# Optimization experiments

Hardware: AMD Instinct MI355X
Metric: run time of the kernel (lower is better)

## Reference

```python
import jax, jax.numpy as jnp
import numpy as np

N = 100000   # nodes
M = N - 1    # tree edges (child -> parent)
EMB = 512    # embedding_size
ENC = 512    # encoder_size


def setup_inputs() -> dict:
    key = jax.random.key(0)
    ks = jax.random.split(key, 10)
    x = jax.random.normal(ks[0], (N, EMB), jnp.float32)
    h = jax.random.normal(ks[1], (N, ENC), jnp.float32)
    c = jax.random.normal(ks[2], (N, ENC), jnp.float32)
    child_idx = jax.random.randint(ks[3], (M,), 0, N)
    parent_idx = jax.random.randint(ks[4], (M,), 0, N)
    s = 0.05
    W_iou = jax.random.normal(ks[5], (3 * ENC, EMB), jnp.float32) * s
    U_iou = jax.random.normal(ks[6], (3 * ENC, ENC), jnp.float32) * s
    b_iou = jnp.zeros((3 * ENC,), jnp.float32)
    U_f_w = jax.random.normal(ks[7], (ENC, ENC), jnp.float32) * s
    U_f_b = jax.random.normal(ks[8], (ENC,), jnp.float32) * s
    return {"x": x, "h": h, "c": c, "child_idx": child_idx,
            "parent_idx": parent_idx, "W_iou": W_iou, "U_iou": U_iou,
            "b_iou": b_iou, "U_f_w": U_f_w, "U_f_b": U_f_b}


def reference(x, h, c, child_idx, parent_idx, W_iou, U_iou, b_iou, U_f_w, U_f_b):
    n = x.shape[0]
    # message_func: gather child states along edges  [M, ENC]
    h_src = h[child_idx]
    c_src = c[child_idx]
    # reduce_func: forget gate per child, ragged sums over children
    f = jax.nn.sigmoid(h_src @ U_f_w.T + U_f_b)               # [M, ENC]
    h_tilde = jax.ops.segment_sum(h_src, parent_idx, num_segments=n)
    c_red = jax.ops.segment_sum(f * c_src, parent_idx, num_segments=n)
    deg = jax.ops.segment_sum(jnp.ones((h_src.shape[0],), x.dtype),
                              parent_idx, num_segments=n)
    has_child = (deg > 0)[:, None]
    # reduce_func overwrites iou with U_iou(h_tilde) for nodes with children;
    # leaves keep the initial W_iou(x).
    iou = jnp.where(has_child, h_tilde @ U_iou.T, x @ W_iou.T) + b_iou
    i, o, u = jnp.split(iou, 3, axis=1)
    c_new = jax.nn.sigmoid(i) * jnp.tanh(u) + jnp.where(has_child, c_red, 0.0)
    h_new = jax.nn.sigmoid(o) * jnp.tanh(c_new)
    return h_new, c_new
```

## Files before the change

### kernel.cpp

```cpp
#include <hip/hip_runtime.h>
#include <stdint.h>

typedef __bf16 bf16x8 __attribute__((ext_vector_type(8)));
typedef float f32x4 __attribute__((ext_vector_type(4)));
typedef unsigned short ushort8 __attribute__((ext_vector_type(8)));

__device__ __forceinline__ float bf2f(unsigned short u) {
  union { uint32_t i; float f; } v; v.i = ((uint32_t)u) << 16; return v.f;
}
__device__ __forceinline__ unsigned short f2bf(float f) {
  union { uint32_t i; float f; } v; v.f = f;
  uint32_t u = v.i;
  return (unsigned short)((u + 0x7fffu + ((u >> 16) & 1u)) >> 16);
}
__device__ __forceinline__ float sigm(float x) { return 1.0f / (1.0f + __expf(-x)); }
__device__ __forceinline__ float tanh_f(float x) { return 1.0f - 2.0f / (__expf(2.0f * x) + 1.0f); }

__device__ __forceinline__ ushort4 cvt4(float4 a) {
  ushort4 o; o.x = f2bf(a.x); o.y = f2bf(a.y); o.z = f2bf(a.z); o.w = f2bf(a.w); return o;
}

__device__ __forceinline__ int xcd_swz(int bid, int nwg) {
  int q = nwg >> 3, r = nwg & 7;
  int x = bid & 7, idx = bid >> 3;
  return (x < r ? x * (q + 1) : r * (q + 1) + (x - r) * q) + idx;
}

__global__ void k_f2bf(const float* __restrict__ src, unsigned short* __restrict__ dst, long long n8) {
  long long t = (long long)blockIdx.x * blockDim.x + threadIdx.x;
  if (t >= n8) return;
  const float4* s = (const float4*)src + t * 2;
  float4 a = s[0], b = s[1];
  ((ushort4*)dst)[t * 2]     = cvt4(a);
  ((ushort4*)dst)[t * 2 + 1] = cvt4(b);
}

__global__ void k_hist(const int* __restrict__ parent, int* __restrict__ deg, int M) {
  int e = blockIdx.x * blockDim.x + threadIdx.x;
  if (e < M) atomicAdd(&deg[parent[e]], 1);
}

__global__ void k_scan1(const int* __restrict__ deg, unsigned long long* __restrict__ ps,
                        unsigned long long* __restrict__ bsum, int Nn) {
  __shared__ unsigned long long tmp[256];
  int t = blockIdx.x * 256 + threadIdx.x;
  int d = (t < Nn) ? deg[t] : 0;
  unsigned long long v = (unsigned long long)(unsigned)d | ((d > 0) ? (1ull << 32) : 0ull);
  tmp[threadIdx.x] = v;
  __syncthreads();
#pragma unroll
  for (int s = 1; s < 256; s <<= 1) {
    unsigned long long a = (threadIdx.x >= (unsigned)s) ? tmp[threadIdx.x - s] : 0;
    __syncthreads();
    tmp[threadIdx.x] += a;
    __syncthreads();
  }
  if (t < Nn) ps[t] = tmp[threadIdx.x] - v;
  if (threadIdx.x == 255) bsum[blockIdx.x] = tmp[255];
}

__global__ void k_scan2(unsigned long long* __restrict__ bsum, int nb,
                        int* __restrict__ meta, int Nn) {
  __shared__ unsigned long long tmp[512];
  int i = threadIdx.x;
  unsigned long long v = (i < nb) ? bsum[i] : 0;
  tmp[i] = v;
  __syncthreads();
#pragma unroll
  for (int s = 1; s < 512; s <<= 1) {
    unsigned long long a = (i >= s) ? tmp[i - s] : 0;
    __syncthreads();
    tmp[i] += a;
    __syncthreads();
  }
  if (i < nb) bsum[i] = tmp[i] - v;
  if (i == 511) {
    int Ni = (int)(tmp[511] >> 32);
    int L0 = ((Ni + 255) >> 8) << 8;
    meta[0] = Ni;
    meta[1] = L0;
    meta[2] = L0 + (Nn - Ni);
  }
}

__global__ void k_scan3(const unsigned long long* __restrict__ ps,
                        const unsigned long long* __restrict__ bsum,
                        const int* __restrict__ meta, const int* __restrict__ deg,
                        int* __restrict__ rs, int* __restrict__ cursor,
                        int* __restrict__ slot, int* __restrict__ nodeof, int Nn) {
  int t = blockIdx.x * 256 + threadIdx.x;
  if (t >= Nn) return;
  unsigned long long p = ps[t] + bsum[blockIdx.x];
  int r  = (int)(p & 0xffffffffull);
  int si = (int)(p >> 32);
  rs[t] = r;
  cursor[t] = r;
  int sl = (deg[t] > 0) ? si : (meta[1] + (t - si));
  slot[t] = sl;
  nodeof[sl] = t;
}

__global__ void k_fill(const int* __restrict__ parent, const int* __restrict__ child,
                       int* __restrict__ cursor, int* __restrict__ childlist, int M) {
  int e = blockIdx.x * blockDim.x + threadIdx.x;
  if (e >= M) return;
  int p = parent[e];
  int pos = atomicAdd(&cursor[p], 1);
  childlist[pos] = child[e];
}

__global__ void k_reduce(const unsigned short* __restrict__ hbuf,
                         const unsigned short* __restrict__ fcb, const float* __restrict__ x,
                         const int* __restrict__ rs, const int* __restrict__ childlist,
                         const int* __restrict__ slot,
                         unsigned short* __restrict__ Zp, unsigned short* __restrict__ credb,
                         int Nn, int M) {
  int p = blockIdx.x * 4 + (threadIdx.x >> 6);
  if (p >= Nn) return;
  int ln = threadIdx.x & 63;
  int j = ln * 8;
  int start = rs[p];
  int end = (p + 1 < Nn) ? rs[p + 1] : M;
  size_t zb = (size_t)slot[p] * 512 + j;
  if (end > start) {
    float hs[8] = {0, 0, 0, 0, 0, 0, 0, 0};
    float cs[8] = {0, 0, 0, 0, 0, 0, 0, 0};
    for (int i = start; i < end; ++i) {
      int ch = childlist[i];
      size_t cb = (size_t)ch * 512 + j;
      ushort8 hv = *(const ushort8*)(hbuf + cb);
      ushort8 fv = *(const ushort8*)(fcb + cb);
#pragma unroll
      for (int q = 0; q < 8; ++q) {
        hs[q] += bf2f(hv[q]);
        cs[q] += bf2f(fv[q]);
      }
    }
    float4 h0 = {hs[0], hs[1], hs[2], hs[3]}, h1 = {hs[4], hs[5], hs[6], hs[7]};
    float4 c0 = {cs[0], cs[1], cs[2], cs[3]}, c1 = {cs[4], cs[5], cs[6], cs[7]};
    ((ushort4*)(Zp + zb))[0] = cvt4(h0);
    ((ushort4*)(Zp + zb))[1] = cvt4(h1);
    size_t cr = (size_t)p * 512 + j;
    ((ushort4*)(credb + cr))[0] = cvt4(c0);
    ((ushort4*)(credb + cr))[1] = cvt4(c1);
  } else {
    const float4* s = (const float4*)(x + (size_t)p * 512 + j);
    float4 x0 = s[0], x1 = s[1];
    ((ushort4*)(Zp + zb))[0] = cvt4(x0);
    ((ushort4*)(Zp + zb))[1] = cvt4(x1);
  }
}

__global__ __launch_bounds__(512)
void k_gemm_f(const unsigned short* __restrict__ A,
              const unsigned short* __restrict__ Bt,
              const float* __restrict__ bias, const float* __restrict__ cmat,
              unsigned short* __restrict__ C, int Mrows) {
  __shared__ __align__(16) unsigned short ldsA[2][256 * 32];
  __shared__ __align__(16) unsigned short ldsB[2][128 * 32];
  const int K = 512, ldc = 512;
  const int tid = threadIdx.x;
  const int wv = tid >> 6, ln = tid & 63;
  const int wr = wv >> 1, wc = wv & 1;
  int wg = xcd_swz(blockIdx.x, gridDim.x);
  int rowp = wg >> 2;
  int colp = wg & 3;
  const int row0 = rowp * 256;
  const int col0 = colp * 128;

  f32x4 acc[4][4] = {};

  auto stage = [&](int buf, int k0) {
#pragma unroll
    for (int rep = 0; rep < 2; ++rep) {
      int cidx = rep * 512 + tid;
      int r  = cidx >> 2;
      int kc = cidx & 3;
      int kp = (kc ^ ((r >> 1) & 3)) * 8;
      int ga = row0 + r; if (ga > Mrows - 1) ga = Mrows - 1;
      const unsigned short* srcA = A + (size_t)ga * K + k0 + kp;
      __builtin_amdgcn_global_load_lds(
          (const __attribute__((address_space(1))) void*)(void*)srcA,
          (__attribute__((address_space(3))) void*)(&ldsA[buf][(size_t)cidx * 8]),
          16, 0, 0);
    }
    {
      int cidx = tid;
      int r  = cidx >> 2;
      int kc = cidx & 3;
      int kp = (kc ^ ((r >> 1) & 3)) * 8;
      const unsigned short* srcB = Bt + (size_t)(col0 + r) * K + k0 + kp;
      __builtin_amdgcn_global_load_lds(
          (const __attribute__((address_space(1))) void*)(void*)srcB,
          (__attribute__((address_space(3))) void*)(&ldsB[buf][(size_t)cidx * 8]),
          16, 0, 0);
    }
  };

  const int kcr = ((ln >> 4) ^ ((ln >> 1) & 3)) * 8;
  auto compute = [&](int buf) {
    bf16x8 af[4], bfr[4];
#pragma unroll
    for (int mi = 0; mi < 4; ++mi)
      af[mi] = *(const bf16x8*)(&ldsA[buf][(size_t)(wr * 64 + mi * 16 + (ln & 15)) * 32 + kcr]);
#pragma unroll
    for (int ni = 0; ni < 4; ++ni)
      bfr[ni] = *(const bf16x8*)(&ldsB[buf][(size_t)(wc * 64 + ni * 16 + (ln & 15)) * 32 + kcr]);
#pragma unroll
    for (int mi = 0; mi < 4; ++mi)
#pragma unroll
      for (int ni = 0; ni < 4; ++ni)
        acc[mi][ni] = __builtin_amdgcn_mfma_f32_16x16x32_bf16(bfr[ni], af[mi], acc[mi][ni], 0, 0, 0);
  };

  stage(0, 0);
  int cur = 0;
#pragma unroll
  for (int kt = 0; kt < 15; ++kt) {
    stage(cur ^ 1, (kt + 1) * 32);
    asm volatile("s_waitcnt vmcnt(3)" ::: "memory");
    __builtin_amdgcn_s_barrier();
    compute(cur);
    __builtin_amdgcn_s_barrier();
    cur ^= 1;
  }
  asm volatile("s_waitcnt vmcnt(0)" ::: "memory");
  __builtin_amdgcn_s_barrier();
  compute(cur);

#pragma unroll
  for (int mi = 0; mi < 4; ++mi) {
    int gm = row0 + wr * 64 + mi * 16 + (ln & 15);
    if (gm >= Mrows) continue;
#pragma unroll
    for (int ni = 0; ni < 4; ++ni) {
      int gn = col0 + wc * 64 + ni * 16 + (ln >> 4) * 4;
      float4 bv = *(const float4*)(bias + gn);
      float4 cv = *(const float4*)(cmat + (size_t)gm * ldc + gn);
      ushort4 o;
      o.x = f2bf(sigm(acc[mi][ni][0] + bv.x) * cv.x);
      o.y = f2bf(sigm(acc[mi][ni][1] + bv.y) * cv.y);
      o.z = f2bf(sigm(acc[mi][ni][2] + bv.z) * cv.z);
      o.w = f2bf(sigm(acc[mi][ni][3] + bv.w) * cv.w);
      *(ushort4*)(C + (size_t)gm * ldc + gn) = o;
    }
  }
}

__global__ __launch_bounds__(512)
void k_gemm_iou(const unsigned short* __restrict__ Zp,
                const unsigned short* __restrict__ Ub,
                const unsigned short* __restrict__ Wb,
                const float* __restrict__ bias,
                const int* __restrict__ meta,
                const int* __restrict__ nodeof,
                unsigned short* __restrict__ C) {
  __shared__ __align__(16) unsigned short ldsA[2][256 * 32];
  __shared__ __align__(16) unsigned short ldsB[2][128 * 32];
  const int K = 512, ldc = 1536;
  const int tid = threadIdx.x;
  const int wv = tid >> 6, ln = tid & 63;
  const int wr = wv >> 1, wc = wv & 1;
  int wg = xcd_swz(blockIdx.x, gridDim.x);
  int rowp = wg / 12;
  int colp = wg - rowp * 12;
  const int row0 = rowp * 256;
  const int col0 = colp * 128;

  const int Ni = meta[0], L0 = meta[1], lim2 = meta[2];
  const bool internal = row0 < L0;
  const int limit = internal ? Ni : lim2;
  if (row0 >= limit) return;
  const unsigned short* __restrict__ Bt = internal ? Ub : Wb;

  f32x4 acc[4][4] = {};

  auto stage = [&](int buf, int k0) {
#pragma unroll
    for (int rep = 0; rep < 2; ++rep) {
      int cidx = rep * 512 + tid;
      int r  = cidx >> 2;
      int kc = cidx & 3;
      int kp = (kc ^ ((r >> 1) & 3)) * 8;
      int ga = row0 + r; if (ga > limit - 1) ga = limit - 1;
      const unsigned short* srcA = Zp + (size_t)ga * K + k0 + kp;
      __builtin_amdgcn_global_load_lds(
          (const __attribute__((address_space(1))) void*)(void*)srcA,
          (__attribute__((address_space(3))) void*)(&ldsA[buf][(size_t)cidx * 8]),
          16, 0, 0);
    }
    {
      int cidx = tid;
      int r  = cidx >> 2;
      int kc = cidx & 3;
      int kp = (kc ^ ((r >> 1) & 3)) * 8;
      const unsigned short* srcB = Bt + (size_t)(col0 + r) * K + k0 + kp;
      __builtin_amdgcn_global_load_lds(
          (const __attribute__((address_space(1))) void*)(void*)srcB,
          (__attribute__((address_space(3))) void*)(&ldsB[buf][(size_t)cidx * 8]),
          16, 0, 0);
    }
  };

  const int kcr = ((ln >> 4) ^ ((ln >> 1) & 3)) * 8;
  auto compute = [&](int buf) {
    bf16x8 af[4], bfr[4];
#pragma unroll
    for (int mi = 0; mi < 4; ++mi)
      af[mi] = *(const bf16x8*)(&ldsA[buf][(size_t)(wr * 64 + mi * 16 + (ln & 15)) * 32 + kcr]);
#pragma unroll
    for (int ni = 0; ni < 4; ++ni)
      bfr[ni] = *(const bf16x8*)(&ldsB[buf][(size_t)(wc * 64 + ni * 16 + (ln & 15)) * 32 + kcr]);
#pragma unroll
    for (int mi = 0; mi < 4; ++mi)
#pragma unroll
      for (int ni = 0; ni < 4; ++ni)
        acc[mi][ni] = __builtin_amdgcn_mfma_f32_16x16x32_bf16(bfr[ni], af[mi], acc[mi][ni], 0, 0, 0);
  };

  stage(0, 0);
  int cur = 0;
#pragma unroll
  for (int kt = 0; kt < 15; ++kt) {
    stage(cur ^ 1, (kt + 1) * 32);
    asm volatile("s_waitcnt vmcnt(3)" ::: "memory");
    __builtin_amdgcn_s_barrier();
    compute(cur);
    __builtin_amdgcn_s_barrier();
    cur ^= 1;
  }
  asm volatile("s_waitcnt vmcnt(0)" ::: "memory");
  __builtin_amdgcn_s_barrier();
  compute(cur);

#pragma unroll
  for (int mi = 0; mi < 4; ++mi) {
    int m = row0 + wr * 64 + mi * 16 + (ln & 15);
    if (m >= limit) continue;
    int node = nodeof[m];
    size_t ob = (size_t)node * ldc;
#pragma unroll
    for (int ni = 0; ni < 4; ++ni) {
      int gn = col0 + wc * 64 + ni * 16 + (ln >> 4) * 4;
      float4 bv = *(const float4*)(bias + gn);
      ushort4 o;
      o.x = f2bf(acc[mi][ni][0] + bv.x);
      o.y = f2bf(acc[mi][ni][1] + bv.y);
      o.z = f2bf(acc[mi][ni][2] + bv.z);
      o.w = f2bf(acc[mi][ni][3] + bv.w);
      *(ushort4*)(C + ob + gn) = o;
    }
  }
}

__global__ void k_epilogue(const unsigned short* __restrict__ iou,
                           const unsigned short* __restrict__ credb,
                           const int* __restrict__ deg,
                           float* __restrict__ out, int Nn) {
  long long t = (long long)blockIdx.x * blockDim.x + threadIdx.x;
  int n = (int)(t >> 6);
  if (n >= Nn) return;
  int j = ((int)t & 63) * 8;
  size_t ib = (size_t)n * 1536;
  ushort4 iv0 = *(const ushort4*)(iou + ib + j);
  ushort4 iv1 = *(const ushort4*)(iou + ib + j + 4);
  ushort4 ov0 = *(const ushort4*)(iou + ib + 512 + j);
  ushort4 ov1 = *(const ushort4*)(iou + ib + 512 + j + 4);
  ushort4 uv0 = *(const ushort4*)(iou + ib + 1024 + j);
  ushort4 uv1 = *(const ushort4*)(iou + ib + 1024 + j + 4);

  float carr[8] = {0, 0, 0, 0, 0, 0, 0, 0};
  if (deg[n] > 0) {
    size_t cr = (size_t)n * 512 + j;
    ushort4 c0 = *(const ushort4*)(credb + cr);
    ushort4 c1 = *(const ushort4*)(credb + cr + 4);
    carr[0] = bf2f(c0.x); carr[1] = bf2f(c0.y); carr[2] = bf2f(c0.z); carr[3] = bf2f(c0.w);
    carr[4] = bf2f(c1.x); carr[5] = bf2f(c1.y); carr[6] = bf2f(c1.z); carr[7] = bf2f(c1.w);
  }

  float iarr[8] = {bf2f(iv0.x), bf2f(iv0.y), bf2f(iv0.z), bf2f(iv0.w),
                   bf2f(iv1.x), bf2f(iv1.y), bf2f(iv1.z), bf2f(iv1.w)};
  float oarr[8] = {bf2f(ov0.x), bf2f(ov0.y), bf2f(ov0.z), bf2f(ov0.w),
                   bf2f(ov1.x), bf2f(ov1.y), bf2f(ov1.z), bf2f(ov1.w)};
  float uarr[8] = {bf2f(uv0.x), bf2f(uv0.y), bf2f(uv0.z), bf2f(uv0.w),
                   bf2f(uv1.x), bf2f(uv1.y), bf2f(uv1.z), bf2f(uv1.w)};
  float hn[8], cn[8];
#pragma unroll
  for (int q = 0; q < 8; ++q) {
    float cc = sigm(iarr[q]) * tanh_f(uarr[q]) + carr[q];
    cn[q] = cc;
    hn[q] = sigm(oarr[q]) * tanh_f(cc);
  }
  size_t hb = (size_t)n * 512 + j;
  size_t cb = (size_t)Nn * 512 + hb;
  *(float4*)(out + hb)     = make_float4(hn[0], hn[1], hn[2], hn[3]);
  *(float4*)(out + hb + 4) = make_float4(hn[4], hn[5], hn[6], hn[7]);
  *(float4*)(out + cb)     = make_float4(cn[0], cn[1], cn[2], cn[3]);
  *(float4*)(out + cb + 4) = make_float4(cn[4], cn[5], cn[6], cn[7]);
}

extern "C" void kernel_launch(void* const* d_in, const int* in_sizes, int n_in,
                              void* d_out, int out_size, void* d_ws, size_t ws_size,
                              hipStream_t stream) {
  const float* x     = (const float*)d_in[0];
  const float* h     = (const float*)d_in[1];
  const float* c     = (const float*)d_in[2];
  const int* child   = (const int*)d_in[3];
  const int* parent  = (const int*)d_in[4];
  const float* W_iou = (const float*)d_in[5];
  const float* U_iou = (const float*)d_in[6];
  const float* b_iou = (const float*)d_in[7];
  const float* U_f_w = (const float*)d_in[8];
  const float* U_f_b = (const float*)d_in[9];

  const int Nn = in_sizes[0] / 512;
  const int M  = in_sizes[3];

  float* out = (float*)d_out;

  char* ws = (char*)d_ws;
  auto al = [](size_t v) { return (v + 255) & ~(size_t)255; };
  size_t sz0    = al((size_t)Nn * 1536 * 2);
  size_t offZp  = sz0;
  size_t szZp   = al((size_t)(Nn + 256) * 512 * 2);
  size_t offHb  = offZp + szZp;
  size_t szHb   = al((size_t)Nn * 512 * 2);
  size_t offCr  = offHb + szHb;
  size_t szCr   = al((size_t)Nn * 512 * 2);
  size_t offDeg = offCr + szCr;
  size_t szN4   = al((size_t)Nn * 4);
  size_t offRs  = offDeg + szN4;
  size_t offCur = offRs + szN4;
  size_t offSl  = offCur + szN4;
  size_t offNo  = offSl + szN4;
  size_t szNo   = al((size_t)(Nn + 256) * 4);
  size_t offPs  = offNo + szNo;
  size_t szPs   = al((size_t)Nn * 8);
  size_t offCl  = offPs + szPs;
  size_t szCl   = al((size_t)M * 4);
  size_t offBs  = offCl + szCl;
  size_t szBs   = al(512 * 8);
  size_t offMt  = offBs + szBs;
  size_t szMt   = 256;
  size_t offWf  = offMt + szMt;
  size_t szWf   = al(512 * 512 * 2);
  size_t offUb  = offWf + szWf;
  size_t szUw   = al((size_t)1536 * 512 * 2);
  size_t offWb  = offUb + szUw;
  size_t needed = offWb + szUw;
  if (ws_size < needed) return;

  unsigned short* fcb   = (unsigned short*)(ws);
  unsigned short* iou   = (unsigned short*)(ws);
  unsigned short* Zp    = (unsigned short*)(ws + offZp);
  unsigned short* hbuf  = (unsigned short*)(ws + offHb);
  unsigned short* credb = (unsigned short*)(ws + offCr);
  int*            deg   = (int*)(ws + offDeg);
  int*            rs    = (int*)(ws + offRs);
  int*            cursor= (int*)(ws + offCur);
  int*            slot  = (int*)(ws + offSl);
  int*            nodeof= (int*)(ws + offNo);
  unsigned long long* ps   = (unsigned long long*)(ws + offPs);
  int*            clist = (int*)(ws + offCl);
  unsigned long long* bsum = (unsigned long long*)(ws + offBs);
  int*            meta  = (int*)(ws + offMt);
  unsigned short* Wf    = (unsigned short*)(ws + offWf);
  unsigned short* Ub    = (unsigned short*)(ws + offUb);
  unsigned short* Wb    = (unsigned short*)(ws + offWb);

  hipMemsetAsync(deg, 0, (size_t)Nn * 4, stream);

  long long n8h = (long long)Nn * 512 / 8;
  k_f2bf<<<(int)((n8h + 255) / 256), 256, 0, stream>>>(h, hbuf, n8h);
  k_f2bf<<<(512 * 512 / 8 + 255) / 256, 256, 0, stream>>>(U_f_w, Wf, 512 * 512 / 8);
  k_f2bf<<<(1536 * 512 / 8 + 255) / 256, 256, 0, stream>>>(U_iou, Ub, 1536 * 512 / 8);
  k_f2bf<<<(1536 * 512 / 8 + 255) / 256, 256, 0, stream>>>(W_iou, Wb, 1536 * 512 / 8);

  int nb1 = (Nn + 255) / 256;
  k_hist<<<(M + 255) / 256, 256, 0, stream>>>(parent, deg, M);
  k_scan1<<<nb1, 256, 0, stream>>>(deg, ps, bsum, Nn);
  k_scan2<<<1, 512, 0, stream>>>(bsum, nb1, meta, Nn);
  k_scan3<<<nb1, 256, 0, stream>>>(ps, bsum, meta, deg, rs, cursor, slot, nodeof, Nn);
  k_fill<<<(M + 255) / 256, 256, 0, stream>>>(parent, child, cursor, clist, M);

  int nbyF = (Nn + 255) / 256;
  k_gemm_f<<<nbyF * 4, 512, 0, stream>>>(hbuf, Wf, U_f_b, c, fcb, Nn);

  k_reduce<<<(Nn + 3) / 4, 256, 0, stream>>>(hbuf, fcb, x, rs, clist, slot, Zp, credb, Nn, M);

  int nbyI = (Nn >> 8) + 2;
  k_gemm_iou<<<nbyI * 12, 512, 0, stream>>>(Zp, Ub, Wb, b_iou, meta, nodeof, iou);

  k_epilogue<<<(int)(((long long)Nn * 64 + 255) / 256), 256, 0, stream>>>(iou, credb, deg, out, Nn);
}
```

Baseline: 710.8 us.

## Fuse LSTM gate epilogue into iou GEMM by looping i, u, o column blocks

Each iou GEMM workgroup now computes the matching i, u and o 128-column blocks one after another, holding the intermediate gate values in registers. It applies sigmoid/tanh and the child-cell sum in-register and writes h and c directly, so the separate epilogue kernel and the bf16 iou round trip through global memory are gone. Reduced c is now stored at the permuted row index so the GEMM can read it in row order. In exchange the grid shrinks to a third of the workgroups, each running three times as many K iterations, with more registers live.

```diff
diff --git a/kernel.cpp b/kernel.cpp
--- a/kernel.cpp
+++ b/kernel.cpp
@@ -140,9 +140,8 @@
     float4 c0 = {cs[0], cs[1], cs[2], cs[3]}, c1 = {cs[4], cs[5], cs[6], cs[7]};
     ((ushort4*)(Zp + zb))[0] = cvt4(h0);
     ((ushort4*)(Zp + zb))[1] = cvt4(h1);
-    size_t cr = (size_t)p * 512 + j;
-    ((ushort4*)(credb + cr))[0] = cvt4(c0);
-    ((ushort4*)(credb + cr))[1] = cvt4(c1);
+    ((ushort4*)(credb + zb))[0] = cvt4(c0);
+    ((ushort4*)(credb + zb))[1] = cvt4(c1);
   } else {
     const float4* s = (const float4*)(x + (size_t)p * 512 + j);
     float4 x0 = s[0], x1 = s[1];
@@ -248,22 +247,23 @@
 }
 
 __global__ __launch_bounds__(512)
-void k_gemm_iou(const unsigned short* __restrict__ Zp,
-                const unsigned short* __restrict__ Ub,
-                const unsigned short* __restrict__ Wb,
-                const float* __restrict__ bias,
-                const int* __restrict__ meta,
-                const int* __restrict__ nodeof,
-                unsigned short* __restrict__ C) {
+void k_gemm_iou_fused(const unsigned short* __restrict__ Zp,
+                      const unsigned short* __restrict__ Ub,
+                      const unsigned short* __restrict__ Wb,
+                      const float* __restrict__ bias,
+                      const int* __restrict__ meta,
+                      const int* __restrict__ nodeof,
+                      const unsigned short* __restrict__ credb,
+                      float* __restrict__ out, int Nn) {
   __shared__ __align__(16) unsigned short ldsA[2][256 * 32];
   __shared__ __align__(16) unsigned short ldsB[2][128 * 32];
-  const int K = 512, ldc = 1536;
+  const int K = 512;
   const int tid = threadIdx.x;
   const int wv = tid >> 6, ln = tid & 63;
   const int wr = wv >> 1, wc = wv & 1;
   int wg = xcd_swz(blockIdx.x, gridDim.x);
-  int rowp = wg / 12;
-  int colp = wg - rowp * 12;
+  int rowp = wg >> 2;
+  int colp = wg & 3;
   const int row0 = rowp * 256;
   const int col0 = colp * 128;
 
@@ -274,8 +274,12 @@
   const unsigned short* __restrict__ Bt = internal ? Ub : Wb;
 
   f32x4 acc[4][4] = {};
-
-  auto stage = [&](int buf, int k0) {
+  ushort4 sto[4][4];
+
+  auto stage = [&](int buf, int s) {
+    int p  = s >> 4;
+    int g  = (2 * p) % 3;
+    int k0 = (s & 15) * 32;
 #pragma unroll
     for (int rep = 0; rep < 2; ++rep) {
       int cidx = rep * 512 + tid;
@@ -294,7 +298,7 @@
       int r  = cidx >> 2;
       int kc = cidx & 3;
       int kp = (kc ^ ((r >> 1) & 3)) * 8;
-      const unsigned short* srcB = Bt + (size_t)(col0 + r) * K + k0 + kp;
+      const unsigned short* srcB = Bt + (size_t)(g * 512 + col0 + r) * K + k0 + kp;
       __builtin_amdgcn_global_load_lds(
           (const __attribute__((address_space(1))) void*)(void*)srcB,
           (__attribute__((address_space(3))) void*)(&ldsB[buf][(size_t)cidx * 8]),
@@ -320,9 +324,64 @@
 
   stage(0, 0);
   int cur = 0;
-#pragma unroll
-  for (int kt = 0; kt < 15; ++kt) {
-    stage(cur ^ 1, (kt + 1) * 32);
+
+#pragma unroll
+  for (int s = 0; s < 16; ++s) {
+    stage(cur ^ 1, s + 1);
+    asm volatile("s_waitcnt vmcnt(3)" ::: "memory");
+    __builtin_amdgcn_s_barrier();
+    compute(cur);
+    __builtin_amdgcn_s_barrier();
+    cur ^= 1;
+  }
+#pragma unroll
+  for (int ni = 0; ni < 4; ++ni) {
+    int gn = col0 + wc * 64 + ni * 16 + (ln >> 4) * 4;
+    float4 bv = *(const float4*)(bias + gn);
+#pragma unroll
+    for (int mi = 0; mi < 4; ++mi) {
+      float4 t;
+      t.x = sigm(acc[mi][ni][0] + bv.x);
+      t.y = sigm(acc[mi][ni][1] + bv.y);
+      t.z = sigm(acc[mi][ni][2] + bv.z);
+      t.w = sigm(acc[mi][ni][3] + bv.w);
+      sto[mi][ni] = cvt4(t);
+      acc[mi][ni] = (f32x4){0.f, 0.f, 0.f, 0.f};
+    }
+  }
+
+#pragma unroll
+  for (int s = 16; s < 32; ++s) {
+    stage(cur ^ 1, s + 1);
+    asm volatile("s_waitcnt vmcnt(3)" ::: "memory");
+    __builtin_amdgcn_s_barrier();
+    compute(cur);
+    __builtin_amdgcn_s_barrier();
+    cur ^= 1;
+  }
+#pragma unroll
+  for (int ni = 0; ni < 4; ++ni) {
+    int gn = col0 + wc * 64 + ni * 16 + (ln >> 4) * 4;
+    float4 bv = *(const float4*)(bias + 1024 + gn);
+#pragma unroll
+    for (int mi = 0; mi < 4; ++mi) {
+      int m = row0 + wr * 64 + mi * 16 + (ln & 15);
+      int mc = (m > limit - 1) ? (limit - 1) : m;
+      ushort4 cr = (ushort4){0, 0, 0, 0};
+      if (internal) cr = *(const ushort4*)(credb + (size_t)mc * 512 + gn);
+      float4 t;
+      t.x = bf2f(sto[mi][ni].x) * tanh_f(acc[mi][ni][0] + bv.x) + bf2f(cr.x);
+      t.y = bf2f(sto[mi][ni].y) * tanh_f(acc[mi][ni][1] + bv.y) + bf2f(cr.y);
+      t.z = bf2f(sto[mi][ni].z) * tanh_f(acc[mi][ni][2] + bv.z) + bf2f(cr.z);
+      t.w = bf2f(sto[mi][ni].w) * tanh_f(acc[mi][ni][3] + bv.w) + bf2f(cr.w);
+      sto[mi][ni] = cvt4(t);
+      acc[mi][ni] = (f32x4){0.f, 0.f, 0.f, 0.f};
+    }
+  }
+
+#pragma unroll
+  for (int s = 32; s < 47; ++s) {
+    stage(cur ^ 1, s + 1);
     asm volatile("s_waitcnt vmcnt(3)" ::: "memory");
     __builtin_amdgcn_s_barrier();
     compute(cur);
@@ -333,70 +392,28 @@
   __builtin_amdgcn_s_barrier();
   compute(cur);
 
+  const size_t cOff = (size_t)Nn * 512;
 #pragma unroll
   for (int mi = 0; mi < 4; ++mi) {
     int m = row0 + wr * 64 + mi * 16 + (ln & 15);
     if (m >= limit) continue;
     int node = nodeof[m];
-    size_t ob = (size_t)node * ldc;
+    size_t hb = (size_t)node * 512;
 #pragma unroll
     for (int ni = 0; ni < 4; ++ni) {
       int gn = col0 + wc * 64 + ni * 16 + (ln >> 4) * 4;
-      float4 bv = *(const float4*)(bias + gn);
-      ushort4 o;
-      o.x = f2bf(acc[mi][ni][0] + bv.x);
-      o.y = f2bf(acc[mi][ni][1] + bv.y);
-      o.z = f2bf(acc[mi][ni][2] + bv.z);
-      o.w = f2bf(acc[mi][ni][3] + bv.w);
-      *(ushort4*)(C + ob + gn) = o;
-    }
-  }
-}
-
-__global__ void k_epilogue(const unsigned short* __restrict__ iou,
-                           const unsigned short* __restrict__ credb,
-                           const int* __restrict__ deg,
-                           float* __restrict__ out, int Nn) {
-  long long t = (long long)blockIdx.x * blockDim.x + threadIdx.x;
-  int n = (int)(t >> 6);
-  if (n >= Nn) return;
-  int j = ((int)t & 63) * 8;
-  size_t ib = (size_t)n * 1536;
-  ushort4 iv0 = *(const ushort4*)(iou + ib + j);
-  ushort4 iv1 = *(const ushort4*)(iou + ib + j + 4);
-  ushort4 ov0 = *(const ushort4*)(iou + ib + 512 + j);
-  ushort4 ov1 = *(const ushort4*)(iou + ib + 512 + j + 4);
-  ushort4 uv0 = *(const ushort4*)(iou + ib + 1024 + j);
-  ushort4 uv1 = *(const ushort4*)(iou + ib + 1024 + j + 4);
-
-  float carr[8] = {0, 0, 0, 0, 0, 0, 0, 0};
-  if (deg[n] > 0) {
-    size_t cr = (size_t)n * 512 + j;
-    ushort4 c0 = *(const ushort4*)(credb + cr);
-    ushort4 c1 = *(const ushort4*)(credb + cr + 4);
-    carr[0] = bf2f(c0.x); carr[1] = bf2f(c0.y); carr[2] = bf2f(c0.z); carr[3] = bf2f(c0.w);
-    carr[4] = bf2f(c1.x); carr[5] = bf2f(c1.y); carr[6] = bf2f(c1.z); carr[7] = bf2f(c1.w);
-  }
-
-  float iarr[8] = {bf2f(iv0.x), bf2f(iv0.y), bf2f(iv0.z), bf2f(iv0.w),
-                   bf2f(iv1.x), bf2f(iv1.y), bf2f(iv1.z), bf2f(iv1.w)};
-  float oarr[8] = {bf2f(ov0.x), bf2f(ov0.y), bf2f(ov0.z), bf2f(ov0.w),
-                   bf2f(ov1.x), bf2f(ov1.y), bf2f(ov1.z), bf2f(ov1.w)};
-  float uarr[8] = {bf2f(uv0.x), bf2f(uv0.y), bf2f(uv0.z), bf2f(uv0.w),
-                   bf2f(uv1.x), bf2f(uv1.y), bf2f(uv1.z), bf2f(uv1.w)};
-  float hn[8], cn[8];
-#pragma unroll
-  for (int q = 0; q < 8; ++q) {
-    float cc = sigm(iarr[q]) * tanh_f(uarr[q]) + carr[q];
-    cn[q] = cc;
-    hn[q] = sigm(oarr[q]) * tanh_f(cc);
-  }
-  size_t hb = (size_t)n * 512 + j;
-  size_t cb = (size_t)Nn * 512 + hb;
-  *(float4*)(out + hb)     = make_float4(hn[0], hn[1], hn[2], hn[3]);
-  *(float4*)(out + hb + 4) = make_float4(hn[4], hn[5], hn[6], hn[7]);
-  *(float4*)(out + cb)     = make_float4(cn[0], cn[1], cn[2], cn[3]);
-  *(float4*)(out + cb + 4) = make_float4(cn[4], cn[5], cn[6], cn[7]);
+      float4 bv = *(const float4*)(bias + 512 + gn);
+      float4 cn, hn;
+      cn.x = bf2f(sto[mi][ni].x); cn.y = bf2f(sto[mi][ni].y);
+      cn.z = bf2f(sto[mi][ni].z); cn.w = bf2f(sto[mi][ni].w);
+      hn.x = sigm(acc[mi][ni][0] + bv.x) * tanh_f(cn.x);
+      hn.y = sigm(acc[mi][ni][1] + bv.y) * tanh_f(cn.y);
+      hn.z = sigm(acc[mi][ni][2] + bv.z) * tanh_f(cn.z);
+      hn.w = sigm(acc[mi][ni][3] + bv.w) * tanh_f(cn.w);
+      *(float4*)(out + hb + gn)        = hn;
+      *(float4*)(out + cOff + hb + gn) = cn;
+    }
+  }
 }
 
 extern "C" void kernel_launch(void* const* d_in, const int* in_sizes, int n_in,
@@ -420,13 +437,13 @@
 
   char* ws = (char*)d_ws;
   auto al = [](size_t v) { return (v + 255) & ~(size_t)255; };
-  size_t sz0    = al((size_t)Nn * 1536 * 2);
-  size_t offZp  = sz0;
+  size_t szFc   = al((size_t)Nn * 512 * 2);
+  size_t offZp  = szFc;
   size_t szZp   = al((size_t)(Nn + 256) * 512 * 2);
   size_t offHb  = offZp + szZp;
   size_t szHb   = al((size_t)Nn * 512 * 2);
   size_t offCr  = offHb + szHb;
-  size_t szCr   = al((size_t)Nn * 512 * 2);
+  size_t szCr   = al((size_t)(Nn + 512) * 512 * 2);
   size_t offDeg = offCr + szCr;
   size_t szN4   = al((size_t)Nn * 4);
   size_t offRs  = offDeg + szN4;
@@ -451,7 +468,6 @@
   if (ws_size < needed) return;
 
   unsigned short* fcb   = (unsigned short*)(ws);
-  unsigned short* iou   = (unsigned short*)(ws);
   unsigned short* Zp    = (unsigned short*)(ws + offZp);
   unsigned short* hbuf  = (unsigned short*)(ws + offHb);
   unsigned short* credb = (unsigned short*)(ws + offCr);
@@ -489,7 +505,5 @@
   k_reduce<<<(Nn + 3) / 4, 256, 0, stream>>>(hbuf, fcb, x, rs, clist, slot, Zp, credb, Nn, M);
 
   int nbyI = (Nn >> 8) + 2;
-  k_gemm_iou<<<nbyI * 12, 512, 0, stream>>>(Zp, Ub, Wb, b_iou, meta, nodeof, iou);
-
-  k_epilogue<<<(int)(((long long)Nn * 64 + 255) / 256), 256, 0, stream>>>(iou, credb, deg, out, Nn);
-}
+  k_gemm_iou_fused<<<nbyI * 4, 512, 0, stream>>>(Zp, Ub, Wb, b_iou, meta, nodeof, credb, out, Nn);
+}
```

New measurement: 861.1 us. 21.1% more time.

## Compact forget-gate GEMM to nodes that appear as children

Applied to the files above, without the earlier changes.

Counts how often each node appears as a child, builds a compacted index of the distinct child nodes with a three-pass scan, and converts only those h rows to bf16. The forget-gate GEMM then runs only over the compacted rows, with blocks past the count exiting early, and reads c through the node map. The reduce gathers through the compact index. With random child indices about a third of the nodes never appear as a child, so this removes that share of the bf16 conversion and forget GEMM work. The cost is extra histogram and scan launches plus one more indirection in the reduce.

```diff
diff --git a/kernel.cpp b/kernel.cpp
--- a/kernel.cpp
+++ b/kernel.cpp
@@ -35,9 +35,9 @@
   ((ushort4*)dst)[t * 2 + 1] = cvt4(b);
 }
 
-__global__ void k_hist(const int* __restrict__ parent, int* __restrict__ deg, int M) {
+__global__ void k_hist(const int* __restrict__ idx, int* __restrict__ cnt, int M) {
   int e = blockIdx.x * blockDim.x + threadIdx.x;
-  if (e < M) atomicAdd(&deg[parent[e]], 1);
+  if (e < M) atomicAdd(&cnt[idx[e]], 1);
 }
 
 __global__ void k_scan1(const int* __restrict__ deg, unsigned long long* __restrict__ ps,
@@ -100,6 +100,57 @@
   nodeof[sl] = t;
 }
 
+__global__ void k_cscan1(const int* __restrict__ chdeg, int* __restrict__ bs2, int Nn) {
+  __shared__ int tmp[256];
+  int t = blockIdx.x * 256 + threadIdx.x;
+  tmp[threadIdx.x] = (t < Nn && chdeg[t] > 0) ? 1 : 0;
+  __syncthreads();
+#pragma unroll
+  for (int s = 128; s > 0; s >>= 1) {
+    if (threadIdx.x < s) tmp[threadIdx.x] += tmp[threadIdx.x + s];
+    __syncthreads();
+  }
+  if (threadIdx.x == 0) bs2[blockIdx.x] = tmp[0];
+}
+
+__global__ void k_cscan2(int* __restrict__ bs2, int nb, int* __restrict__ meta) {
+  __shared__ int tmp[512];
+  int i = threadIdx.x;
+  int v = (i < nb) ? bs2[i] : 0;
+  tmp[i] = v;
+  __syncthreads();
+#pragma unroll
+  for (int s = 1; s < 512; s <<= 1) {
+    int a = (i >= s) ? tmp[i - s] : 0;
+    __syncthreads();
+    tmp[i] += a;
+    __syncthreads();
+  }
+  if (i < nb) bs2[i] = tmp[i] - v;
+  if (i == 511) meta[3] = tmp[511];
+}
+
+__global__ void k_cscan3(const int* __restrict__ chdeg, const int* __restrict__ bs2,
+                         int* __restrict__ cidx, int* __restrict__ cnodes, int Nn) {
+  __shared__ int tmp[256];
+  int t = blockIdx.x * 256 + threadIdx.x;
+  int v = (t < Nn && chdeg[t] > 0) ? 1 : 0;
+  tmp[threadIdx.x] = v;
+  __syncthreads();
+#pragma unroll
+  for (int s = 1; s < 256; s <<= 1) {
+    int a = (threadIdx.x >= s) ? tmp[threadIdx.x - s] : 0;
+    __syncthreads();
+    tmp[threadIdx.x] += a;
+    __syncthreads();
+  }
+  if (t < Nn) {
+    int ci = tmp[threadIdx.x] - v + bs2[blockIdx.x];
+    cidx[t] = ci;
+    if (v) cnodes[ci] = t;
+  }
+}
+
 __global__ void k_fill(const int* __restrict__ parent, const int* __restrict__ child,
                        int* __restrict__ cursor, int* __restrict__ childlist, int M) {
   int e = blockIdx.x * blockDim.x + threadIdx.x;
@@ -109,10 +160,24 @@
   childlist[pos] = child[e];
 }
 
-__global__ void k_reduce(const unsigned short* __restrict__ hbuf,
-                         const unsigned short* __restrict__ fcb, const float* __restrict__ x,
+__global__ void k_h2bf_compact(const float* __restrict__ h, const int* __restrict__ chdeg,
+                               const int* __restrict__ cidx,
+                               unsigned short* __restrict__ hbufc, int Nn) {
+  long long t = (long long)blockIdx.x * blockDim.x + threadIdx.x;
+  int n = (int)(t >> 6);
+  if (n >= Nn) return;
+  if (chdeg[n] == 0) return;
+  int j = ((int)t & 63) * 8;
+  const float4* s = (const float4*)(h + (size_t)n * 512 + j);
+  size_t d = (size_t)cidx[n] * 512 + j;
+  ((ushort4*)(hbufc + d))[0] = cvt4(s[0]);
+  ((ushort4*)(hbufc + d))[1] = cvt4(s[1]);
+}
+
+__global__ void k_reduce(const unsigned short* __restrict__ hbufc,
+                         const unsigned short* __restrict__ fcc, const float* __restrict__ x,
                          const int* __restrict__ rs, const int* __restrict__ childlist,
-                         const int* __restrict__ slot,
+                         const int* __restrict__ slot, const int* __restrict__ cidx,
                          unsigned short* __restrict__ Zp, unsigned short* __restrict__ credb,
                          int Nn, int M) {
   int p = blockIdx.x * 4 + (threadIdx.x >> 6);
@@ -127,9 +192,10 @@
     float cs[8] = {0, 0, 0, 0, 0, 0, 0, 0};
     for (int i = start; i < end; ++i) {
       int ch = childlist[i];
-      size_t cb = (size_t)ch * 512 + j;
-      ushort8 hv = *(const ushort8*)(hbuf + cb);
-      ushort8 fv = *(const ushort8*)(fcb + cb);
+      int ri = cidx[ch];
+      size_t cb = (size_t)ri * 512 + j;
+      ushort8 hv = *(const ushort8*)(hbufc + cb);
+      ushort8 fv = *(const ushort8*)(fcc + cb);
 #pragma unroll
       for (int q = 0; q < 8; ++q) {
         hs[q] += bf2f(hv[q]);
@@ -155,7 +221,8 @@
 void k_gemm_f(const unsigned short* __restrict__ A,
               const unsigned short* __restrict__ Bt,
               const float* __restrict__ bias, const float* __restrict__ cmat,
-              unsigned short* __restrict__ C, int Mrows) {
+              const int* __restrict__ meta, const int* __restrict__ cnodes,
+              unsigned short* __restrict__ C) {
   __shared__ __align__(16) unsigned short ldsA[2][256 * 32];
   __shared__ __align__(16) unsigned short ldsB[2][128 * 32];
   const int K = 512, ldc = 512;
@@ -167,32 +234,34 @@
   int colp = wg & 3;
   const int row0 = rowp * 256;
   const int col0 = colp * 128;
+  const int Mc = meta[3];
+  if (row0 >= Mc) return;
 
   f32x4 acc[4][4] = {};
 
   auto stage = [&](int buf, int k0) {
 #pragma unroll
     for (int rep = 0; rep < 2; ++rep) {
-      int cidx = rep * 512 + tid;
-      int r  = cidx >> 2;
-      int kc = cidx & 3;
+      int cidx2 = rep * 512 + tid;
+      int r  = cidx2 >> 2;
+      int kc = cidx2 & 3;
       int kp = (kc ^ ((r >> 1) & 3)) * 8;
-      int ga = row0 + r; if (ga > Mrows - 1) ga = Mrows - 1;
+      int ga = row0 + r; if (ga > Mc - 1) ga = Mc - 1;
       const unsigned short* srcA = A + (size_t)ga * K + k0 + kp;
       __builtin_amdgcn_global_load_lds(
           (const __attribute__((address_space(1))) void*)(void*)srcA,
-          (__attribute__((address_space(3))) void*)(&ldsA[buf][(size_t)cidx * 8]),
+          (__attribute__((address_space(3))) void*)(&ldsA[buf][(size_t)cidx2 * 8]),
           16, 0, 0);
     }
     {
-      int cidx = tid;
-      int r  = cidx >> 2;
-      int kc = cidx & 3;
+      int cidx2 = tid;
+      int r  = cidx2 >> 2;
+      int kc = cidx2 & 3;
       int kp = (kc ^ ((r >> 1) & 3)) * 8;
       const unsigned short* srcB = Bt + (size_t)(col0 + r) * K + k0 + kp;
       __builtin_amdgcn_global_load_lds(
           (const __attribute__((address_space(1))) void*)(void*)srcB,
-          (__attribute__((address_space(3))) void*)(&ldsB[buf][(size_t)cidx * 8]),
+          (__attribute__((address_space(3))) void*)(&ldsB[buf][(size_t)cidx2 * 8]),
           16, 0, 0);
     }
   };
@@ -231,12 +300,13 @@
 #pragma unroll
   for (int mi = 0; mi < 4; ++mi) {
     int gm = row0 + wr * 64 + mi * 16 + (ln & 15);
-    if (gm >= Mrows) continue;
+    if (gm >= Mc) continue;
+    int node = cnodes[gm];
 #pragma unroll
     for (int ni = 0; ni < 4; ++ni) {
       int gn = col0 + wc * 64 + ni * 16 + (ln >> 4) * 4;
       float4 bv = *(const float4*)(bias + gn);
-      float4 cv = *(const float4*)(cmat + (size_t)gm * ldc + gn);
+      float4 cv = *(const float4*)(cmat + (size_t)node * ldc + gn);
       ushort4 o;
       o.x = f2bf(sigm(acc[mi][ni][0] + bv.x) * cv.x);
       o.y = f2bf(sigm(acc[mi][ni][1] + bv.y) * cv.y);
@@ -278,26 +348,26 @@
   auto stage = [&](int buf, int k0) {
 #pragma unroll
     for (int rep = 0; rep < 2; ++rep) {
-      int cidx = rep * 512 + tid;
-      int r  = cidx >> 2;
-      int kc = cidx & 3;
+      int cidx2 = rep * 512 + tid;
+      int r  = cidx2 >> 2;
+      int kc = cidx2 & 3;
       int kp = (kc ^ ((r >> 1) & 3)) * 8;
       int ga = row0 + r; if (ga > limit - 1) ga = limit - 1;
       const unsigned short* srcA = Zp + (size_t)ga * K + k0 + kp;
       __builtin_amdgcn_global_load_lds(
           (const __attribute__((address_space(1))) void*)(void*)srcA,
-          (__attribute__((address_space(3))) void*)(&ldsA[buf][(size_t)cidx * 8]),
+          (__attribute__((address_space(3))) void*)(&ldsA[buf][(size_t)cidx2 * 8]),
           16, 0, 0);
     }
     {
-      int cidx = tid;
-      int r  = cidx >> 2;
-      int kc = cidx & 3;
+      int cidx2 = tid;
+      int r  = cidx2 >> 2;
+      int kc = cidx2 & 3;
       int kp = (kc ^ ((r >> 1) & 3)) * 8;
       const unsigned short* srcB = Bt + (size_t)(col0 + r) * K + k0 + kp;
       __builtin_amdgcn_global_load_lds(
           (const __attribute__((address_space(1))) void*)(void*)srcB,
-          (__attribute__((address_space(3))) void*)(&ldsB[buf][(size_t)cidx * 8]),
+          (__attribute__((address_space(3))) void*)(&ldsB[buf][(size_t)cidx2 * 8]),
           16, 0, 0);
     }
   };
@@ -429,18 +499,23 @@
   size_t szCr   = al((size_t)Nn * 512 * 2);
   size_t offDeg = offCr + szCr;
   size_t szN4   = al((size_t)Nn * 4);
-  size_t offRs  = offDeg + szN4;
+  size_t offChd = offDeg + szN4;
+  size_t offRs  = offChd + szN4;
   size_t offCur = offRs + szN4;
   size_t offSl  = offCur + szN4;
   size_t offNo  = offSl + szN4;
   size_t szNo   = al((size_t)(Nn + 256) * 4);
-  size_t offPs  = offNo + szNo;
+  size_t offCi  = offNo + szNo;
+  size_t offCn  = offCi + szN4;
+  size_t offPs  = offCn + szN4;
   size_t szPs   = al((size_t)Nn * 8);
   size_t offCl  = offPs + szPs;
   size_t szCl   = al((size_t)M * 4);
   size_t offBs  = offCl + szCl;
   size_t szBs   = al(512 * 8);
-  size_t offMt  = offBs + szBs;
+  size_t offBs2 = offBs + szBs;
+  size_t szBs2  = al(512 * 4);
+  size_t offMt  = offBs2 + szBs2;
   size_t szMt   = 256;
   size_t offWf  = offMt + szMt;
   size_t szWf   = al(512 * 512 * 2);
@@ -450,43 +525,51 @@
   size_t needed = offWb + szUw;
   if (ws_size < needed) return;
 
-  unsigned short* fcb   = (unsigned short*)(ws);
+  unsigned short* fcc   = (unsigned short*)(ws);
   unsigned short* iou   = (unsigned short*)(ws);
   unsigned short* Zp    = (unsigned short*)(ws + offZp);
-  unsigned short* hbuf  = (unsigned short*)(ws + offHb);
+  unsigned short* hbufc = (unsigned short*)(ws + offHb);
   unsigned short* credb = (unsigned short*)(ws + offCr);
   int*            deg   = (int*)(ws + offDeg);
+  int*            chdeg = (int*)(ws + offChd);
   int*            rs    = (int*)(ws + offRs);
   int*            cursor= (int*)(ws + offCur);
   int*            slot  = (int*)(ws + offSl);
   int*            nodeof= (int*)(ws + offNo);
+  int*            cidx  = (int*)(ws + offCi);
+  int*            cnodes= (int*)(ws + offCn);
   unsigned long long* ps   = (unsigned long long*)(ws + offPs);
   int*            clist = (int*)(ws + offCl);
   unsigned long long* bsum = (unsigned long long*)(ws + offBs);
+  int*            bs2   = (int*)(ws + offBs2);
   int*            meta  = (int*)(ws + offMt);
   unsigned short* Wf    = (unsigned short*)(ws + offWf);
   unsigned short* Ub    = (unsigned short*)(ws + offUb);
   unsigned short* Wb    = (unsigned short*)(ws + offWb);
 
-  hipMemsetAsync(deg, 0, (size_t)Nn * 4, stream);
-
-  long long n8h = (long long)Nn * 512 / 8;
-  k_f2bf<<<(int)((n8h + 255) / 256), 256, 0, stream>>>(h, hbuf, n8h);
+  hipMemsetAsync(deg, 0, 2 * szN4, stream);
+
   k_f2bf<<<(512 * 512 / 8 + 255) / 256, 256, 0, stream>>>(U_f_w, Wf, 512 * 512 / 8);
   k_f2bf<<<(1536 * 512 / 8 + 255) / 256, 256, 0, stream>>>(U_iou, Ub, 1536 * 512 / 8);
   k_f2bf<<<(1536 * 512 / 8 + 255) / 256, 256, 0, stream>>>(W_iou, Wb, 1536 * 512 / 8);
 
   int nb1 = (Nn + 255) / 256;
   k_hist<<<(M + 255) / 256, 256, 0, stream>>>(parent, deg, M);
+  k_hist<<<(M + 255) / 256, 256, 0, stream>>>(child, chdeg, M);
   k_scan1<<<nb1, 256, 0, stream>>>(deg, ps, bsum, Nn);
   k_scan2<<<1, 512, 0, stream>>>(bsum, nb1, meta, Nn);
   k_scan3<<<nb1, 256, 0, stream>>>(ps, bsum, meta, deg, rs, cursor, slot, nodeof, Nn);
   k_fill<<<(M + 255) / 256, 256, 0, stream>>>(parent, child, cursor, clist, M);
+  k_cscan1<<<nb1, 256, 0, stream>>>(chdeg, bs2, Nn);
+  k_cscan2<<<1, 512, 0, stream>>>(bs2, nb1, meta);
+  k_cscan3<<<nb1, 256, 0, stream>>>(chdeg, bs2, cidx, cnodes, Nn);
+
+  k_h2bf_compact<<<(int)(((long long)Nn * 64 + 255) / 256), 256, 0, stream>>>(h, chdeg, cidx, hbufc, Nn);
 
   int nbyF = (Nn + 255) / 256;
-  k_gemm_f<<<nbyF * 4, 512, 0, stream>>>(hbuf, Wf, U_f_b, c, fcb, Nn);
-
-  k_reduce<<<(Nn + 3) / 4, 256, 0, stream>>>(hbuf, fcb, x, rs, clist, slot, Zp, credb, Nn, M);
+  k_gemm_f<<<nbyF * 4, 512, 0, stream>>>(hbufc, Wf, U_f_b, c, meta, cnodes, fcc);
+
+  k_reduce<<<(Nn + 3) / 4, 256, 0, stream>>>(hbufc, fcc, x, rs, clist, slot, cidx, Zp, credb, Nn, M);
 
   int nbyI = (Nn >> 8) + 2;
   k_gemm_iou<<<nbyI * 12, 512, 0, stream>>>(Zp, Ub, Wb, b_iou, meta, nodeof, iou);
```

New measurement: 698.0 us. No clear change (-1.8%).
